# Optimization experiments

Hardware: AMD Instinct MI355X
Metric: run time of the kernel (lower is better)

Reference implementation:

```python
import jax, jax.numpy as jnp
import numpy as np

B, KEY, D, U, MODES = 16384, 64, 128, 128, 32

def setup_inputs() -> dict:
    key = jax.random.key(0)
    k1, k2, k3, k4, k5 = jax.random.split(key, 5)
    return {
        "key": jax.random.normal(k1, (B, KEY), dtype=jnp.float32),
        "x": jax.random.normal(k2, (B, D), dtype=jnp.float32),
        "sens": jnp.ones((MODES,), dtype=jnp.float32),
        "keys_map": jax.random.normal(k3, (MODES, KEY), dtype=jnp.float32),
        "kernels": jax.random.normal(k4, (MODES, D, U), dtype=jnp.float32) * 0.05,
        "biases": jax.random.normal(k5, (MODES, U), dtype=jnp.float32) * 0.05,
    }

def reference(key, x, sens, keys_map, kernels, biases):
    # key: [B, KEY]; keys_map: [MODES, KEY]
    # Euclidean distance of each key to each mode's stored key.
    dist = jnp.sqrt(jnp.sum((key[:, None, :] - keys_map[None, :, :]) ** 2, axis=-1))  # [B, MODES]
    sim = jax.nn.softmax(sens / (dist + 1.0), axis=-1)  # [B, MODES]
    modes = kernels.shape[0]
    # Original: kernel_b = mean_m(sim[b,m] * kernels[m]); out_b = x_b @ kernel_b.
    # Reordered as GEMM-per-mode + weighted combine (same math):
    out = jnp.einsum('bm,bd,mdu->bu', sim, x, kernels) / modes  # [B, U]
    out = out + (sim @ biases) / modes  # mean over modes of sim-weighted biases
    return out
```

## Files before the change

### kernel.cpp

```cpp
#include <hip/hip_runtime.h>

#define BATCH 16384
#define KEYD  64
#define DDIM  128
#define UDIM  128
#define MODES 32

typedef __attribute__((ext_vector_type(8))) short bf16x8;
typedef __attribute__((ext_vector_type(4))) float f32x4;

__device__ __forceinline__ unsigned short f2bf(float f) {
  unsigned u = __float_as_uint(f);
  unsigned r = (u + 0x7FFFu + ((u >> 16) & 1u)) >> 16;
  return (unsigned short)r;
}

__device__ __forceinline__ void gld_lds16(const void* g, void* l) {
  __builtin_amdgcn_global_load_lds(
      (const __attribute__((address_space(1))) unsigned int*)g,
      (__attribute__((address_space(3))) unsigned int*)l, 16, 0, 0);
}

__global__ __launch_bounds__(256) void prep_sim_x(
    const float* __restrict__ key, const float* __restrict__ x,
    const float* __restrict__ sens, const float* __restrict__ keys_map,
    float* __restrict__ sim, unsigned short* __restrict__ x16) {
  __shared__ float kmT[KEYD * MODES];
  __shared__ float kr[16][KEYD];
  const int t = threadIdx.x;
  for (int i = t; i < MODES * KEYD; i += 256) {
    int m = i >> 6, k = i & 63;
    kmT[k * MODES + m] = keys_map[i];
  }
  {
    const float4 v = *(const float4*)(key + (long)blockIdx.x * 16 * KEYD + t * 4);
    *(float4*)(&kr[0][0] + t * 4) = v;
  }
  __syncthreads();

  const int lane = t & 63, wave = t >> 6;
  const int half = lane >> 5, m = lane & 31;
  const float sv = sens[m];

  #pragma unroll
  for (int pass = 0; pass < 2; ++pass) {
    const int rl = pass * 8 + wave * 2 + half;
    const long row = (long)blockIdx.x * 16 + rl;

    float d2 = 0.f;
    #pragma unroll
    for (int k = 0; k < KEYD; ++k) {
      float diff = kr[rl][k] - kmT[k * MODES + m];
      d2 += diff * diff;
    }
    float logit = sv / (sqrtf(d2) + 1.0f);
    float mx = logit;
    #pragma unroll
    for (int off = 16; off > 0; off >>= 1) mx = fmaxf(mx, __shfl_xor(mx, off, 64));
    float e = __expf(logit - mx);
    float s = e;
    #pragma unroll
    for (int off = 16; off > 0; off >>= 1) s += __shfl_xor(s, off, 64);
    sim[row * MODES + m] = e / s;

    const float4 xv = *(const float4*)(x + row * DDIM + m * 4);
    ushort4 o;
    o.x = f2bf(xv.x); o.y = f2bf(xv.y); o.z = f2bf(xv.z); o.w = f2bf(xv.w);
    *(ushort4*)(x16 + row * DDIM + m * 4) = o;
  }
}

__global__ __launch_bounds__(256) void prep_wb(
    const float* __restrict__ kernels, const float* __restrict__ biases,
    unsigned short* __restrict__ kb16, unsigned short* __restrict__ bb16) {
  int t = blockIdx.x * 256 + threadIdx.x;
  if (t < MODES * 16 * UDIM) {
    int u = t & 127, kb = (t >> 7) & 15, m = t >> 11;
    const float* src = kernels + (long)((m * 16 + kb) * 8) * UDIM + u;
    ushort4 lo, hi;
    lo.x = f2bf(src[0 * UDIM]); lo.y = f2bf(src[1 * UDIM]);
    lo.z = f2bf(src[2 * UDIM]); lo.w = f2bf(src[3 * UDIM]);
    hi.x = f2bf(src[4 * UDIM]); hi.y = f2bf(src[5 * UDIM]);
    hi.z = f2bf(src[6 * UDIM]); hi.w = f2bf(src[7 * UDIM]);
    *(ushort4*)(kb16 + (long)t * 8) = lo;
    *(ushort4*)(kb16 + (long)t * 8 + 4) = hi;
  } else if (t < MODES * 16 * UDIM + 4 * UDIM) {
    int tb = t - MODES * 16 * UDIM;
    int u = tb & 127, kb = tb >> 7;
    const float* src = biases + kb * 8 * UDIM + u;
    ushort4 lo, hi;
    lo.x = f2bf(src[0 * UDIM]); lo.y = f2bf(src[1 * UDIM]);
    lo.z = f2bf(src[2 * UDIM]); lo.w = f2bf(src[3 * UDIM]);
    hi.x = f2bf(src[4 * UDIM]); hi.y = f2bf(src[5 * UDIM]);
    hi.z = f2bf(src[6 * UDIM]); hi.w = f2bf(src[7 * UDIM]);
    *(ushort4*)(bb16 + (long)tb * 8) = lo;
    *(ushort4*)(bb16 + (long)tb * 8 + 4) = hi;
  }
}

__global__ __launch_bounds__(256, 2) void gemm_poly(
    const unsigned short* __restrict__ x16, const unsigned short* __restrict__ kb16,
    const unsigned short* __restrict__ bb16, const float* __restrict__ sim,
    float* __restrict__ out) {
  __shared__ alignas(16) unsigned short bsh[2][16 * UDIM * 8];
  __shared__ alignas(16) float simT[8][128];

  const int t = threadIdx.x;
  const int lane = t & 63, w = t >> 6;
  const int q = lane >> 4, l16 = lane & 15;
  const int wrow = (w >> 1) * 64, wcol = (w & 1) * 64;
  const long bm = (long)blockIdx.x * 128;
  const int split = blockIdx.y;

  {
    int rrow = t >> 1, mg = (t & 1) * 4;
    const float4 v = *(const float4*)(sim + (bm + rrow) * MODES + split * 8 + mg);
    simT[mg + 0][rrow] = v.x; simT[mg + 1][rrow] = v.y;
    simT[mg + 2][rrow] = v.z; simT[mg + 3][rrow] = v.w;
  }

  bf16x8 aF[4][4];
  #pragma unroll
  for (int rt = 0; rt < 4; ++rt)
    #pragma unroll
    for (int ks = 0; ks < 4; ++ks)
      aF[rt][ks] = *(const bf16x8*)(x16 + (bm + wrow + rt * 16 + l16) * DDIM + ks * 32 + q * 8);

  const unsigned short* kbase = kb16 + (long)(split * 8) * (16 * UDIM * 8);
  #pragma unroll
  for (int i = 0; i < 8; ++i) {
    int off = (t + i * 256) * 8;
    gld_lds16(kbase + off, &bsh[0][off]);
  }

  f32x4 acc[4][4] = {};

  for (int mi = 0; mi < 8; ++mi) {
    __syncthreads();
    if (mi < 7) {
      const unsigned short* src = kbase + (long)(mi + 1) * (16 * UDIM * 8);
      unsigned short* dst = bsh[(mi + 1) & 1];
      #pragma unroll
      for (int i = 0; i < 8; ++i) {
        int off = (t + i * 256) * 8;
        gld_lds16(src + off, dst + off);
      }
    }

    const unsigned short* bs = bsh[mi & 1];
    bf16x8 bF[4][4];
    #pragma unroll
    for (int ks = 0; ks < 4; ++ks)
      #pragma unroll
      for (int ct = 0; ct < 4; ++ct)
        bF[ks][ct] = *(const bf16x8*)&bs[(((ks * 4 + q) * UDIM) + wcol + ct * 16 + l16) * 8];

    #pragma unroll
    for (int rt = 0; rt < 4; ++rt) {
      f32x4 tmp[4] = {};
      #pragma unroll
      for (int ks = 0; ks < 4; ++ks)
        #pragma unroll
        for (int ct = 0; ct < 4; ++ct)
          tmp[ct] = __builtin_amdgcn_mfma_f32_16x16x32_bf16(aF[rt][ks], bF[ks][ct], tmp[ct], 0, 0, 0);
      const f32x4 s = *(const f32x4*)&simT[mi][wrow + rt * 16 + q * 4];
      #pragma unroll
      for (int ct = 0; ct < 4; ++ct)
        acc[rt][ct] += s * tmp[ct];
    }
  }

  if (split == 0) {
    bf16x8 sF[4];
    #pragma unroll
    for (int rt = 0; rt < 4; ++rt) {
      const float* sp = sim + (bm + wrow + rt * 16 + l16) * MODES + q * 8;
      bf16x8 f;
      #pragma unroll
      for (int j = 0; j < 8; ++j) f[j] = (short)f2bf(sp[j]);
      sF[rt] = f;
    }
    #pragma unroll
    for (int ct = 0; ct < 4; ++ct) {
      bf16x8 bb = *(const bf16x8*)(bb16 + (long)(q * UDIM + wcol + ct * 16 + l16) * 8);
      #pragma unroll
      for (int rt = 0; rt < 4; ++rt)
        acc[rt][ct] = __builtin_amdgcn_mfma_f32_16x16x32_bf16(sF[rt], bb, acc[rt][ct], 0, 0, 0);
    }
  }

  #pragma unroll
  for (int rt = 0; rt < 4; ++rt)
    #pragma unroll
    for (int ct = 0; ct < 4; ++ct) {
      long row = bm + wrow + rt * 16 + q * 4;
      int col = wcol + ct * 16 + l16;
      #pragma unroll
      for (int r = 0; r < 4; ++r)
        atomicAdd(out + (row + r) * UDIM + col, acc[rt][ct][r] * (1.0f / MODES));
    }
}

extern "C" void kernel_launch(void* const* d_in, const int* in_sizes, int n_in,
                              void* d_out, int out_size, void* d_ws, size_t ws_size,
                              hipStream_t stream) {
  const float* key      = (const float*)d_in[0];
  const float* x        = (const float*)d_in[1];
  const float* sens     = (const float*)d_in[2];
  const float* keys_map = (const float*)d_in[3];
  const float* kernels  = (const float*)d_in[4];
  const float* biases   = (const float*)d_in[5];
  float* out = (float*)d_out;

  char* ws = (char*)d_ws;
  float*          sim  = (float*)ws;
  unsigned short* x16  = (unsigned short*)(ws + (2u << 20));
  unsigned short* kb16 = (unsigned short*)(ws + (6u << 20));
  unsigned short* bb16 = (unsigned short*)(ws + (7u << 20));

  hipMemsetAsync(out, 0, (size_t)BATCH * UDIM * sizeof(float), stream);
  prep_sim_x<<<BATCH / 16, 256, 0, stream>>>(key, x, sens, keys_map, sim, x16);
  prep_wb<<<(MODES * 16 * UDIM + 4 * UDIM + 255) / 256, 256, 0, stream>>>(kernels, biases, kb16, bb16);
  gemm_poly<<<dim3(BATCH / 128, 4), 256, 0, stream>>>(x16, kb16, bb16, sim, out);
}
```

Measured before the change: 129.0 us.

## Fuse prep kernels with output zeroing and read GEMM weights directly from global

The memset and the two prep kernels are merged into one launch: the first 1024 blocks zero the output, compute the softmax similarities and convert x to bf16, and the remaining blocks convert the weights and biases. The GEMM drops its LDS double-buffered weight staging and loads B fragments straight from global memory, relying on cache hits. It also splits the output columns across twice as many blocks, with each wave now handling 32 rows, and raises launch bounds to 3 blocks per CU. This cuts launch overhead and register and LDS pressure to raise occupancy, at the cost of more atomic traffic and redundant loads of x and the weights.

```diff
diff --git a/kernel.cpp b/kernel.cpp
--- a/kernel.cpp
+++ b/kernel.cpp
@@ -15,102 +15,102 @@
   return (unsigned short)r;
 }
 
-__device__ __forceinline__ void gld_lds16(const void* g, void* l) {
-  __builtin_amdgcn_global_load_lds(
-      (const __attribute__((address_space(1))) unsigned int*)g,
-      (__attribute__((address_space(3))) unsigned int*)l, 16, 0, 0);
-}
-
-__global__ __launch_bounds__(256) void prep_sim_x(
+__global__ __launch_bounds__(256) void prep_all(
     const float* __restrict__ key, const float* __restrict__ x,
     const float* __restrict__ sens, const float* __restrict__ keys_map,
-    float* __restrict__ sim, unsigned short* __restrict__ x16) {
+    const float* __restrict__ kernels, const float* __restrict__ biases,
+    float* __restrict__ sim, unsigned short* __restrict__ x16,
+    unsigned short* __restrict__ kb16, unsigned short* __restrict__ bb16,
+    float* __restrict__ out) {
+  const int t = threadIdx.x;
+  const int bid = blockIdx.x;
+
   __shared__ float kmT[KEYD * MODES];
   __shared__ float kr[16][KEYD];
-  const int t = threadIdx.x;
-  for (int i = t; i < MODES * KEYD; i += 256) {
-    int m = i >> 6, k = i & 63;
-    kmT[k * MODES + m] = keys_map[i];
-  }
-  {
-    const float4 v = *(const float4*)(key + (long)blockIdx.x * 16 * KEYD + t * 4);
-    *(float4*)(&kr[0][0] + t * 4) = v;
-  }
-  __syncthreads();
-
-  const int lane = t & 63, wave = t >> 6;
-  const int half = lane >> 5, m = lane & 31;
-  const float sv = sens[m];
-
-  #pragma unroll
-  for (int pass = 0; pass < 2; ++pass) {
-    const int rl = pass * 8 + wave * 2 + half;
-    const long row = (long)blockIdx.x * 16 + rl;
-
-    float d2 = 0.f;
-    #pragma unroll
-    for (int k = 0; k < KEYD; ++k) {
-      float diff = kr[rl][k] - kmT[k * MODES + m];
-      d2 += diff * diff;
-    }
-    float logit = sv / (sqrtf(d2) + 1.0f);
-    float mx = logit;
-    #pragma unroll
-    for (int off = 16; off > 0; off >>= 1) mx = fmaxf(mx, __shfl_xor(mx, off, 64));
-    float e = __expf(logit - mx);
-    float s = e;
-    #pragma unroll
-    for (int off = 16; off > 0; off >>= 1) s += __shfl_xor(s, off, 64);
-    sim[row * MODES + m] = e / s;
-
-    const float4 xv = *(const float4*)(x + row * DDIM + m * 4);
-    ushort4 o;
-    o.x = f2bf(xv.x); o.y = f2bf(xv.y); o.z = f2bf(xv.z); o.w = f2bf(xv.w);
-    *(ushort4*)(x16 + row * DDIM + m * 4) = o;
-  }
-}
-
-__global__ __launch_bounds__(256) void prep_wb(
-    const float* __restrict__ kernels, const float* __restrict__ biases,
-    unsigned short* __restrict__ kb16, unsigned short* __restrict__ bb16) {
-  int t = blockIdx.x * 256 + threadIdx.x;
-  if (t < MODES * 16 * UDIM) {
-    int u = t & 127, kb = (t >> 7) & 15, m = t >> 11;
-    const float* src = kernels + (long)((m * 16 + kb) * 8) * UDIM + u;
-    ushort4 lo, hi;
-    lo.x = f2bf(src[0 * UDIM]); lo.y = f2bf(src[1 * UDIM]);
-    lo.z = f2bf(src[2 * UDIM]); lo.w = f2bf(src[3 * UDIM]);
-    hi.x = f2bf(src[4 * UDIM]); hi.y = f2bf(src[5 * UDIM]);
-    hi.z = f2bf(src[6 * UDIM]); hi.w = f2bf(src[7 * UDIM]);
-    *(ushort4*)(kb16 + (long)t * 8) = lo;
-    *(ushort4*)(kb16 + (long)t * 8 + 4) = hi;
-  } else if (t < MODES * 16 * UDIM + 4 * UDIM) {
-    int tb = t - MODES * 16 * UDIM;
-    int u = tb & 127, kb = tb >> 7;
-    const float* src = biases + kb * 8 * UDIM + u;
-    ushort4 lo, hi;
-    lo.x = f2bf(src[0 * UDIM]); lo.y = f2bf(src[1 * UDIM]);
-    lo.z = f2bf(src[2 * UDIM]); lo.w = f2bf(src[3 * UDIM]);
-    hi.x = f2bf(src[4 * UDIM]); hi.y = f2bf(src[5 * UDIM]);
-    hi.z = f2bf(src[6 * UDIM]); hi.w = f2bf(src[7 * UDIM]);
-    *(ushort4*)(bb16 + (long)tb * 8) = lo;
-    *(ushort4*)(bb16 + (long)tb * 8 + 4) = hi;
-  }
-}
-
-__global__ __launch_bounds__(256, 2) void gemm_poly(
+
+  if (bid < BATCH / 16) {
+    const float4 z = make_float4(0.f, 0.f, 0.f, 0.f);
+    float4* op = (float4*)out + (long)bid * 512;
+    op[t] = z; op[t + 256] = z;
+
+    for (int i = t; i < MODES * KEYD; i += 256) {
+      int m = i >> 6, k = i & 63;
+      kmT[k * MODES + m] = keys_map[i];
+    }
+    *(float4*)(&kr[0][0] + t * 4) =
+        *(const float4*)(key + (long)bid * 16 * KEYD + t * 4);
+    __syncthreads();
+
+    const int lane = t & 63, wave = t >> 6;
+    const int half = lane >> 5, m = lane & 31;
+    const float sv = sens[m];
+
+    #pragma unroll
+    for (int pass = 0; pass < 2; ++pass) {
+      const int rl = pass * 8 + wave * 2 + half;
+      const long row = (long)bid * 16 + rl;
+
+      float d2 = 0.f;
+      #pragma unroll
+      for (int k = 0; k < KEYD; ++k) {
+        float diff = kr[rl][k] - kmT[k * MODES + m];
+        d2 += diff * diff;
+      }
+      float logit = sv / (sqrtf(d2) + 1.0f);
+      float mx = logit;
+      #pragma unroll
+      for (int off = 16; off > 0; off >>= 1) mx = fmaxf(mx, __shfl_xor(mx, off, 64));
+      float e = __expf(logit - mx);
+      float s = e;
+      #pragma unroll
+      for (int off = 16; off > 0; off >>= 1) s += __shfl_xor(s, off, 64);
+      sim[row * MODES + m] = e / s;
+
+      const float4 xv = *(const float4*)(x + row * DDIM + m * 4);
+      ushort4 o;
+      o.x = f2bf(xv.x); o.y = f2bf(xv.y); o.z = f2bf(xv.z); o.w = f2bf(xv.w);
+      *(ushort4*)(x16 + row * DDIM + m * 4) = o;
+    }
+  } else {
+    int tt = (bid - BATCH / 16) * 256 + t;
+    if (tt < MODES * 16 * UDIM) {
+      int u = tt & 127, kb = (tt >> 7) & 15, m = tt >> 11;
+      const float* src = kernels + (long)((m * 16 + kb) * 8) * UDIM + u;
+      ushort4 lo, hi;
+      lo.x = f2bf(src[0 * UDIM]); lo.y = f2bf(src[1 * UDIM]);
+      lo.z = f2bf(src[2 * UDIM]); lo.w = f2bf(src[3 * UDIM]);
+      hi.x = f2bf(src[4 * UDIM]); hi.y = f2bf(src[5 * UDIM]);
+      hi.z = f2bf(src[6 * UDIM]); hi.w = f2bf(src[7 * UDIM]);
+      *(ushort4*)(kb16 + (long)tt * 8) = lo;
+      *(ushort4*)(kb16 + (long)tt * 8 + 4) = hi;
+    } else {
+      int tb = tt - MODES * 16 * UDIM;
+      int u = tb & 127, kb = tb >> 7;
+      const float* src = biases + kb * 8 * UDIM + u;
+      ushort4 lo, hi;
+      lo.x = f2bf(src[0 * UDIM]); lo.y = f2bf(src[1 * UDIM]);
+      lo.z = f2bf(src[2 * UDIM]); lo.w = f2bf(src[3 * UDIM]);
+      hi.x = f2bf(src[4 * UDIM]); hi.y = f2bf(src[5 * UDIM]);
+      hi.z = f2bf(src[6 * UDIM]); hi.w = f2bf(src[7 * UDIM]);
+      *(ushort4*)(bb16 + (long)tb * 8) = lo;
+      *(ushort4*)(bb16 + (long)tb * 8 + 4) = hi;
+    }
+  }
+}
+
+__global__ __launch_bounds__(256, 3) void gemm_poly(
     const unsigned short* __restrict__ x16, const unsigned short* __restrict__ kb16,
     const unsigned short* __restrict__ bb16, const float* __restrict__ sim,
     float* __restrict__ out) {
-  __shared__ alignas(16) unsigned short bsh[2][16 * UDIM * 8];
   __shared__ alignas(16) float simT[8][128];
 
   const int t = threadIdx.x;
   const int lane = t & 63, w = t >> 6;
   const int q = lane >> 4, l16 = lane & 15;
-  const int wrow = (w >> 1) * 64, wcol = (w & 1) * 64;
+  const int wrow = w * 32;
   const long bm = (long)blockIdx.x * 128;
-  const int split = blockIdx.y;
+  const int split = blockIdx.y & 3;
+  const int c0 = (blockIdx.y >> 2) * 64;
 
   {
     int rrow = t >> 1, mg = (t & 1) * 4;
@@ -118,45 +118,30 @@
     simT[mg + 0][rrow] = v.x; simT[mg + 1][rrow] = v.y;
     simT[mg + 2][rrow] = v.z; simT[mg + 3][rrow] = v.w;
   }
-
-  bf16x8 aF[4][4];
+  __syncthreads();
+
+  bf16x8 aF[2][4];
   #pragma unroll
-  for (int rt = 0; rt < 4; ++rt)
+  for (int rt = 0; rt < 2; ++rt)
     #pragma unroll
     for (int ks = 0; ks < 4; ++ks)
       aF[rt][ks] = *(const bf16x8*)(x16 + (bm + wrow + rt * 16 + l16) * DDIM + ks * 32 + q * 8);
 
+  f32x4 acc[2][4] = {};
   const unsigned short* kbase = kb16 + (long)(split * 8) * (16 * UDIM * 8);
+
   #pragma unroll
-  for (int i = 0; i < 8; ++i) {
-    int off = (t + i * 256) * 8;
-    gld_lds16(kbase + off, &bsh[0][off]);
-  }
-
-  f32x4 acc[4][4] = {};
-
   for (int mi = 0; mi < 8; ++mi) {
-    __syncthreads();
-    if (mi < 7) {
-      const unsigned short* src = kbase + (long)(mi + 1) * (16 * UDIM * 8);
-      unsigned short* dst = bsh[(mi + 1) & 1];
-      #pragma unroll
-      for (int i = 0; i < 8; ++i) {
-        int off = (t + i * 256) * 8;
-        gld_lds16(src + off, dst + off);
-      }
-    }
-
-    const unsigned short* bs = bsh[mi & 1];
+    const unsigned short* mb = kbase + (long)mi * (16 * UDIM * 8);
     bf16x8 bF[4][4];
     #pragma unroll
     for (int ks = 0; ks < 4; ++ks)
       #pragma unroll
       for (int ct = 0; ct < 4; ++ct)
-        bF[ks][ct] = *(const bf16x8*)&bs[(((ks * 4 + q) * UDIM) + wcol + ct * 16 + l16) * 8];
-
-    #pragma unroll
-    for (int rt = 0; rt < 4; ++rt) {
+        bF[ks][ct] = *(const bf16x8*)(mb + ((ks * 4 + q) * UDIM + c0 + ct * 16 + l16) * 8);
+
+    #pragma unroll
+    for (int rt = 0; rt < 2; ++rt) {
       f32x4 tmp[4] = {};
       #pragma unroll
       for (int ks = 0; ks < 4; ++ks)
@@ -171,9 +156,9 @@
   }
 
   if (split == 0) {
-    bf16x8 sF[4];
-    #pragma unroll
-    for (int rt = 0; rt < 4; ++rt) {
+    bf16x8 sF[2];
+    #pragma unroll
+    for (int rt = 0; rt < 2; ++rt) {
       const float* sp = sim + (bm + wrow + rt * 16 + l16) * MODES + q * 8;
       bf16x8 f;
       #pragma unroll
@@ -182,19 +167,19 @@
     }
     #pragma unroll
     for (int ct = 0; ct < 4; ++ct) {
-      bf16x8 bb = *(const bf16x8*)(bb16 + (long)(q * UDIM + wcol + ct * 16 + l16) * 8);
-      #pragma unroll
-      for (int rt = 0; rt < 4; ++rt)
+      bf16x8 bb = *(const bf16x8*)(bb16 + (long)(q * UDIM + c0 + ct * 16 + l16) * 8);
+      #pragma unroll
+      for (int rt = 0; rt < 2; ++rt)
         acc[rt][ct] = __builtin_amdgcn_mfma_f32_16x16x32_bf16(sF[rt], bb, acc[rt][ct], 0, 0, 0);
     }
   }
 
   #pragma unroll
-  for (int rt = 0; rt < 4; ++rt)
+  for (int rt = 0; rt < 2; ++rt)
     #pragma unroll
     for (int ct = 0; ct < 4; ++ct) {
       long row = bm + wrow + rt * 16 + q * 4;
-      int col = wcol + ct * 16 + l16;
+      int col = c0 + ct * 16 + l16;
       #pragma unroll
       for (int r = 0; r < 4; ++r)
         atomicAdd(out + (row + r) * UDIM + col, acc[rt][ct][r] * (1.0f / MODES));
@@ -218,8 +203,7 @@
   unsigned short* kb16 = (unsigned short*)(ws + (6u << 20));
   unsigned short* bb16 = (unsigned short*)(ws + (7u << 20));
 
-  hipMemsetAsync(out, 0, (size_t)BATCH * UDIM * sizeof(float), stream);
-  prep_sim_x<<<BATCH / 16, 256, 0, stream>>>(key, x, sens, keys_map, sim, x16);
-  prep_wb<<<(MODES * 16 * UDIM + 4 * UDIM + 255) / 256, 256, 0, stream>>>(kernels, biases, kb16, bb16);
-  gemm_poly<<<dim3(BATCH / 128, 4), 256, 0, stream>>>(x16, kb16, bb16, sim, out);
-}
+  prep_all<<<BATCH / 16 + 258, 256, 0, stream>>>(
+      key, x, sens, keys_map, kernels, biases, sim, x16, kb16, bb16, out);
+  gemm_poly<<<dim3(BATCH / 128, 8), 256, 0, stream>>>(x16, kb16, bb16, sim, out);
+}
```

Measured after the change: 161.1 us. +24.9%, slower.

## Merge prep kernels and replace atomic output accumulation with partial buffers plus reduce

Applied to the files above, without the earlier changes.

The two preprocessing kernels become one launch. In the sim path, keys_map is held in registers and the distance is split across lane halves, with 32 rows handled per block. The GEMM now writes per-split partial results to a workspace buffer instead of using atomicAdd, and a new reduce kernel sums the four partials and scales them. This removes the memset and the atomic contention on the output, at the cost of 32 MB of extra partial writes and reads plus one extra launch.

```diff
diff --git a/kernel.cpp b/kernel.cpp
--- a/kernel.cpp
+++ b/kernel.cpp
@@ -21,87 +21,94 @@
       (__attribute__((address_space(3))) unsigned int*)l, 16, 0, 0);
 }
 
-__global__ __launch_bounds__(256) void prep_sim_x(
+__global__ __launch_bounds__(256) void prep_all(
     const float* __restrict__ key, const float* __restrict__ x,
     const float* __restrict__ sens, const float* __restrict__ keys_map,
-    float* __restrict__ sim, unsigned short* __restrict__ x16) {
-  __shared__ float kmT[KEYD * MODES];
-  __shared__ float kr[16][KEYD];
+    const float* __restrict__ kernels, const float* __restrict__ biases,
+    float* __restrict__ sim, unsigned short* __restrict__ x16,
+    unsigned short* __restrict__ kb16, unsigned short* __restrict__ bb16) {
   const int t = threadIdx.x;
-  for (int i = t; i < MODES * KEYD; i += 256) {
-    int m = i >> 6, k = i & 63;
-    kmT[k * MODES + m] = keys_map[i];
-  }
-  {
-    const float4 v = *(const float4*)(key + (long)blockIdx.x * 16 * KEYD + t * 4);
-    *(float4*)(&kr[0][0] + t * 4) = v;
-  }
-  __syncthreads();
-
-  const int lane = t & 63, wave = t >> 6;
-  const int half = lane >> 5, m = lane & 31;
-  const float sv = sens[m];
-
-  #pragma unroll
-  for (int pass = 0; pass < 2; ++pass) {
-    const int rl = pass * 8 + wave * 2 + half;
-    const long row = (long)blockIdx.x * 16 + rl;
-
-    float d2 = 0.f;
-    #pragma unroll
-    for (int k = 0; k < KEYD; ++k) {
-      float diff = kr[rl][k] - kmT[k * MODES + m];
-      d2 += diff * diff;
-    }
-    float logit = sv / (sqrtf(d2) + 1.0f);
-    float mx = logit;
-    #pragma unroll
-    for (int off = 16; off > 0; off >>= 1) mx = fmaxf(mx, __shfl_xor(mx, off, 64));
-    float e = __expf(logit - mx);
-    float s = e;
-    #pragma unroll
-    for (int off = 16; off > 0; off >>= 1) s += __shfl_xor(s, off, 64);
-    sim[row * MODES + m] = e / s;
-
-    const float4 xv = *(const float4*)(x + row * DDIM + m * 4);
-    ushort4 o;
-    o.x = f2bf(xv.x); o.y = f2bf(xv.y); o.z = f2bf(xv.z); o.w = f2bf(xv.w);
-    *(ushort4*)(x16 + row * DDIM + m * 4) = o;
-  }
-}
-
-__global__ __launch_bounds__(256) void prep_wb(
-    const float* __restrict__ kernels, const float* __restrict__ biases,
-    unsigned short* __restrict__ kb16, unsigned short* __restrict__ bb16) {
-  int t = blockIdx.x * 256 + threadIdx.x;
-  if (t < MODES * 16 * UDIM) {
-    int u = t & 127, kb = (t >> 7) & 15, m = t >> 11;
-    const float* src = kernels + (long)((m * 16 + kb) * 8) * UDIM + u;
-    ushort4 lo, hi;
-    lo.x = f2bf(src[0 * UDIM]); lo.y = f2bf(src[1 * UDIM]);
-    lo.z = f2bf(src[2 * UDIM]); lo.w = f2bf(src[3 * UDIM]);
-    hi.x = f2bf(src[4 * UDIM]); hi.y = f2bf(src[5 * UDIM]);
-    hi.z = f2bf(src[6 * UDIM]); hi.w = f2bf(src[7 * UDIM]);
-    *(ushort4*)(kb16 + (long)t * 8) = lo;
-    *(ushort4*)(kb16 + (long)t * 8 + 4) = hi;
-  } else if (t < MODES * 16 * UDIM + 4 * UDIM) {
-    int tb = t - MODES * 16 * UDIM;
-    int u = tb & 127, kb = tb >> 7;
-    const float* src = biases + kb * 8 * UDIM + u;
-    ushort4 lo, hi;
-    lo.x = f2bf(src[0 * UDIM]); lo.y = f2bf(src[1 * UDIM]);
-    lo.z = f2bf(src[2 * UDIM]); lo.w = f2bf(src[3 * UDIM]);
-    hi.x = f2bf(src[4 * UDIM]); hi.y = f2bf(src[5 * UDIM]);
-    hi.z = f2bf(src[6 * UDIM]); hi.w = f2bf(src[7 * UDIM]);
-    *(ushort4*)(bb16 + (long)tb * 8) = lo;
-    *(ushort4*)(bb16 + (long)tb * 8 + 4) = hi;
+  const int bid = blockIdx.x;
+
+  if (bid < BATCH / 32) {
+    __shared__ float kr[32][KEYD];
+    *(float4*)(&kr[0][0] + t * 4) =
+        *(const float4*)(key + (long)bid * 32 * KEYD + t * 4);
+    *(float4*)(&kr[0][0] + 1024 + t * 4) =
+        *(const float4*)(key + (long)bid * 32 * KEYD + 1024 + t * 4);
+
+    const int lane = t & 63, wave = t >> 6;
+    const int m = lane & 31, h = lane >> 5;
+    float kreg[32];
+    {
+      const float* kmp = keys_map + m * KEYD + h * 32;
+      #pragma unroll
+      for (int j = 0; j < 32; j += 4) {
+        const float4 v = *(const float4*)(kmp + j);
+        kreg[j] = v.x; kreg[j + 1] = v.y; kreg[j + 2] = v.z; kreg[j + 3] = v.w;
+      }
+    }
+    const float sv = sens[m];
+    __syncthreads();
+
+    #pragma unroll
+    for (int rr = 0; rr < 8; ++rr) {
+      const int rl = wave * 8 + rr;
+      const long row = (long)bid * 32 + rl;
+
+      float d2h = 0.f;
+      #pragma unroll
+      for (int j = 0; j < 32; j += 2) {
+        const float2 kv = *(const float2*)(&kr[rl][h * 32 + j]);
+        float a = kv.x - kreg[j], b = kv.y - kreg[j + 1];
+        d2h += a * a + b * b;
+      }
+      float d2 = d2h + __shfl_xor(d2h, 32, 64);
+      float logit = sv / (sqrtf(d2) + 1.0f);
+      float mx = logit;
+      #pragma unroll
+      for (int off = 16; off > 0; off >>= 1) mx = fmaxf(mx, __shfl_xor(mx, off, 64));
+      float e = __expf(logit - mx);
+      float s = e;
+      #pragma unroll
+      for (int off = 16; off > 0; off >>= 1) s += __shfl_xor(s, off, 64);
+      if (h == 0) sim[row * MODES + m] = e / s;
+
+      const float2 xv = *(const float2*)(x + row * DDIM + lane * 2);
+      ushort2 o; o.x = f2bf(xv.x); o.y = f2bf(xv.y);
+      *(ushort2*)(x16 + row * DDIM + lane * 2) = o;
+    }
+  } else {
+    int tt = (bid - BATCH / 32) * 256 + t;
+    if (tt < MODES * 16 * UDIM) {
+      int u = tt & 127, kb = (tt >> 7) & 15, m = tt >> 11;
+      const float* src = kernels + (long)((m * 16 + kb) * 8) * UDIM + u;
+      ushort4 lo, hi;
+      lo.x = f2bf(src[0 * UDIM]); lo.y = f2bf(src[1 * UDIM]);
+      lo.z = f2bf(src[2 * UDIM]); lo.w = f2bf(src[3 * UDIM]);
+      hi.x = f2bf(src[4 * UDIM]); hi.y = f2bf(src[5 * UDIM]);
+      hi.z = f2bf(src[6 * UDIM]); hi.w = f2bf(src[7 * UDIM]);
+      *(ushort4*)(kb16 + (long)tt * 8) = lo;
+      *(ushort4*)(kb16 + (long)tt * 8 + 4) = hi;
+    } else {
+      int tb = tt - MODES * 16 * UDIM;
+      int u = tb & 127, kb = tb >> 7;
+      const float* src = biases + kb * 8 * UDIM + u;
+      ushort4 lo, hi;
+      lo.x = f2bf(src[0 * UDIM]); lo.y = f2bf(src[1 * UDIM]);
+      lo.z = f2bf(src[2 * UDIM]); lo.w = f2bf(src[3 * UDIM]);
+      hi.x = f2bf(src[4 * UDIM]); hi.y = f2bf(src[5 * UDIM]);
+      hi.z = f2bf(src[6 * UDIM]); hi.w = f2bf(src[7 * UDIM]);
+      *(ushort4*)(bb16 + (long)tb * 8) = lo;
+      *(ushort4*)(bb16 + (long)tb * 8 + 4) = hi;
+    }
   }
 }
 
 __global__ __launch_bounds__(256, 2) void gemm_poly(
     const unsigned short* __restrict__ x16, const unsigned short* __restrict__ kb16,
     const unsigned short* __restrict__ bb16, const float* __restrict__ sim,
-    float* __restrict__ out) {
+    float* __restrict__ partial) {
   __shared__ alignas(16) unsigned short bsh[2][16 * UDIM * 8];
   __shared__ alignas(16) float simT[8][128];
 
@@ -189,6 +196,7 @@
     }
   }
 
+  float* part = partial + (long)split * ((long)BATCH * UDIM);
   #pragma unroll
   for (int rt = 0; rt < 4; ++rt)
     #pragma unroll
@@ -197,8 +205,19 @@
       int col = wcol + ct * 16 + l16;
       #pragma unroll
       for (int r = 0; r < 4; ++r)
-        atomicAdd(out + (row + r) * UDIM + col, acc[rt][ct][r] * (1.0f / MODES));
-    }
+        part[(row + r) * UDIM + col] = acc[rt][ct][r];
+    }
+}
+
+__global__ __launch_bounds__(256) void reduce_parts(
+    const float* __restrict__ partial, float* __restrict__ out) {
+  const long i = ((long)blockIdx.x * 256 + threadIdx.x) * 4;
+  const long S = (long)BATCH * UDIM;
+  const f32x4 p0 = *(const f32x4*)(partial + i);
+  const f32x4 p1 = *(const f32x4*)(partial + S + i);
+  const f32x4 p2 = *(const f32x4*)(partial + 2 * S + i);
+  const f32x4 p3 = *(const f32x4*)(partial + 3 * S + i);
+  *(f32x4*)(out + i) = (p0 + p1 + p2 + p3) * (1.0f / MODES);
 }
 
 extern "C" void kernel_launch(void* const* d_in, const int* in_sizes, int n_in,
@@ -217,9 +236,10 @@
   unsigned short* x16  = (unsigned short*)(ws + (2u << 20));
   unsigned short* kb16 = (unsigned short*)(ws + (6u << 20));
   unsigned short* bb16 = (unsigned short*)(ws + (7u << 20));
-
-  hipMemsetAsync(out, 0, (size_t)BATCH * UDIM * sizeof(float), stream);
-  prep_sim_x<<<BATCH / 16, 256, 0, stream>>>(key, x, sens, keys_map, sim, x16);
-  prep_wb<<<(MODES * 16 * UDIM + 4 * UDIM + 255) / 256, 256, 0, stream>>>(kernels, biases, kb16, bb16);
-  gemm_poly<<<dim3(BATCH / 128, 4), 256, 0, stream>>>(x16, kb16, bb16, sim, out);
-}
+  float*          part = (float*)(ws + (8u << 20));
+
+  prep_all<<<BATCH / 32 + 258, 256, 0, stream>>>(
+      key, x, sens, keys_map, kernels, biases, sim, x16, kb16, bb16);
+  gemm_poly<<<dim3(BATCH / 128, 4), 256, 0, stream>>>(x16, kb16, bb16, sim, part);
+  reduce_parts<<<(BATCH * UDIM) / (256 * 4), 256, 0, stream>>>(part, out);
+}
```

New measurement: 107.9 us. 16.3% less time.
